# Performance work log

Measured on AMD Instinct MI355X. Metric: run time of the kernel, lower is better.

## Reference

```python
import jax, jax.numpy as jnp
import numpy as np

NUM_LAYERS = 5
EMB = 300
BN_EPS = 1e-5


def setup_inputs() -> dict:
    key = jax.random.key(0)
    ks = jax.random.split(key, 16)
    N, E, G = 50000, 800000, 512
    node_feats = jax.random.normal(ks[0], (N, EMB), dtype=jnp.float32)
    src = jax.random.randint(ks[1], (E,), 0, N, dtype=jnp.int32)
    dst = jax.random.randint(ks[2], (E,), 0, N, dtype=jnp.int32)
    graph_ids = jnp.sort(jax.random.randint(ks[3], (N,), 0, G, dtype=jnp.int32))
    L = NUM_LAYERS
    s1 = 1.0 / np.sqrt(EMB)
    s2 = 1.0 / np.sqrt(2 * EMB)
    W1 = jax.random.uniform(ks[4], (L, EMB, 2 * EMB), jnp.float32, -s1, s1)
    b1 = jax.random.uniform(ks[5], (L, 2 * EMB), jnp.float32, -s1, s1)
    W2 = jax.random.uniform(ks[6], (L, 2 * EMB, EMB), jnp.float32, -s2, s2)
    b2 = jax.random.uniform(ks[7], (L, EMB), jnp.float32, -s2, s2)
    eps = jnp.zeros((L,), dtype=jnp.float32)
    gamma = jnp.ones((L, EMB), dtype=jnp.float32)
    beta = jnp.zeros((L, EMB), dtype=jnp.float32)
    return {"node_feats": node_feats, "W1": W1, "b1": b1, "W2": W2, "b2": b2,
            "eps": eps, "gamma": gamma, "beta": beta,
            "src": src, "dst": dst, "graph_ids": graph_ids, "num_graphs": G}


def _batch_norm(x, g, b):
    mu = jnp.mean(x, axis=0)
    var = jnp.var(x, axis=0)
    return (x - mu) * jax.lax.rsqrt(var + BN_EPS) * g + b


def reference(node_feats, W1, b1, W2, b2, eps, gamma, beta, src, dst, graph_ids, num_graphs):
    N = node_feats.shape[0]
    h = node_feats
    for l in range(NUM_LAYERS):
        # message passing: sum of source-node feats at each destination
        neigh = jax.ops.segment_sum(h[src], dst, num_segments=N)  # [N, EMB]
        h = (1.0 + eps[l]) * h + neigh
        h = jax.nn.relu(h @ W1[l] + b1[l]) @ W2[l] + b2[l]
        h = _batch_norm(h, gamma[l], beta[l])
        if l < NUM_LAYERS - 1:
            h = jax.nn.relu(h)
        # dropout is identity in eval mode
    # JK='last' then mean readout per graph
    sums = jax.ops.segment_sum(h, graph_ids, num_segments=num_graphs)  # [G, EMB]
    cnt = jax.ops.segment_sum(jnp.ones((N,), h.dtype), graph_ids, num_segments=num_graphs)
    return sums / jnp.maximum(cnt, 1.0)[:, None]
```

## Files before the change

### kernel.cpp

```cpp
#include <hip/hip_runtime.h>
#include <hip/hip_bf16.h>
#include <stdint.h>

#define EMB 300
#define D1 320
#define D2 640
#define NLAYER 5

typedef __attribute__((ext_vector_type(8))) short short8v;
typedef __attribute__((ext_vector_type(4))) float f32x4;

__device__ __forceinline__ float bf2f(ushort u){
  union { uint32_t i; float f; } c; c.i = ((uint32_t)u) << 16; return c.f;
}
__device__ __forceinline__ ushort f2bf(float f){
  union { float f; uint32_t i; } c; c.f = f;
  uint32_t i = c.i;
  return (ushort)((i + 0x7FFFu + ((i >> 16) & 1u)) >> 16);
}

__global__ void k_prep_w1(const float* __restrict__ W1, ushort* __restrict__ W1H,
                          ushort* __restrict__ W1L){
  int id = blockIdx.x * 256 + threadIdx.x;
  if (id >= NLAYER * D2 * D1) return;
  int l = id / (D2 * D1), r = id % (D2 * D1);
  int n = r / D1, k = r % D1;
  float v = (n < 2*EMB && k < EMB) ? W1[((size_t)l * EMB + k) * (2*EMB) + n] : 0.f;
  ushort hi = f2bf(v);
  W1H[id] = hi;
  W1L[id] = f2bf(v - bf2f(hi));
}
__global__ void k_prep_w2(const float* __restrict__ W2, ushort* __restrict__ W2H,
                          ushort* __restrict__ W2L){
  int id = blockIdx.x * 256 + threadIdx.x;
  if (id >= NLAYER * D1 * D2) return;
  int l = id / (D1 * D2), r = id % (D1 * D2);
  int n = r / D2, k = r % D2;
  float v = (n < EMB && k < 2*EMB) ? W2[((size_t)l * (2*EMB) + k) * EMB + n] : 0.f;
  ushort hi = f2bf(v);
  W2H[id] = hi;
  W2L[id] = f2bf(v - bf2f(hi));
}
__global__ void k_prep_vec(const float* b1, const float* b2, const float* gamma, const float* beta,
                           float* b1p, float* b2p, float* gp, float* bp, float* scsh0){
  int id = blockIdx.x * 256 + threadIdx.x;
  if (id < NLAYER * D2){
    int l = id / D2, n = id % D2;
    b1p[id] = (n < 2*EMB) ? b1[l * (2*EMB) + n] : 0.f;
  }
  if (id < NLAYER * D1){
    int l = id / D1, c = id % D1;
    b2p[id] = (c < EMB) ? b2[l * EMB + c]    : 0.f;
    gp[id]  = (c < EMB) ? gamma[l * EMB + c] : 0.f;
    bp[id]  = (c < EMB) ? beta[l * EMB + c]  : 0.f;
  }
  if (id < D1){
    scsh0[id] = 1.0f;
    scsh0[D1 + id] = 0.0f;
  }
}
__global__ void k_hinit(const float* __restrict__ nf, float* __restrict__ z,
                        ushort* __restrict__ zbf, int N){
  int id = blockIdx.x * 256 + threadIdx.x;
  if (id >= N * 80) return;
  int n = id / 80, q = id % 80;
  float4 v = make_float4(0.f, 0.f, 0.f, 0.f);
  if (q < 75) v = *(const float4*)(nf + (size_t)n * EMB + q * 4);
  *(float4*)(z + (size_t)n * D1 + q * 4) = v;
  ushort o[4] = {f2bf(v.x), f2bf(v.y), f2bf(v.z), f2bf(v.w)};
  *(uint2*)(zbf + (size_t)n * D1 + q * 4) = *(const uint2*)o;
}

__global__ void k_count(const int* __restrict__ dst, int* __restrict__ deg, int E){
  int e = blockIdx.x * 256 + threadIdx.x;
  if (e < E) atomicAdd(&deg[dst[e]], 1);
}
__global__ __launch_bounds__(1024) void k_scan(const int* __restrict__ deg,
                                               int* __restrict__ row_ptr,
                                               int* __restrict__ cursor, int N){
  __shared__ int wsum[16];
  __shared__ int carryS;
  int tid = threadIdx.x, lane = tid & 63, wid = tid >> 6;
  if (tid == 0) carryS = 0;
  __syncthreads();
  for (int base = 0; base < N; base += 1024){
    int i = base + tid;
    int v = (i < N) ? deg[i] : 0;
    int isc = v;
    #pragma unroll
    for (int off = 1; off < 64; off <<= 1){
      int t = __shfl_up(isc, off, 64);
      if (lane >= off) isc += t;
    }
    if (lane == 63) wsum[wid] = isc;
    __syncthreads();
    int woff = 0;
    for (int ww = 0; ww < wid; ww++) woff += wsum[ww];
    int carry = carryS;
    int excl = carry + woff + isc - v;
    if (i < N){ row_ptr[i] = excl; cursor[i] = excl; }
    __syncthreads();
    if (tid == 0){
      int s = 0;
      for (int ww = 0; ww < 16; ww++) s += wsum[ww];
      carryS = carry + s;
    }
    __syncthreads();
  }
  if (tid == 0) row_ptr[N] = carryS;
}
__global__ void k_scatter(const int* __restrict__ src, const int* __restrict__ dst,
                          int* __restrict__ cursor, int* __restrict__ ssrc, int E){
  int e = blockIdx.x * 256 + threadIdx.x;
  if (e < E){
    int p = atomicAdd(&cursor[dst[e]], 1);
    ssrc[p] = src[e];
  }
}

__global__ __launch_bounds__(320) void k_aggregate(const float* __restrict__ z,
                                                   const ushort* __restrict__ zbf,
                                                   const float* __restrict__ scsh,
                                                   ushort* __restrict__ xh,
                                                   ushort* __restrict__ xl,
                                                   const int* __restrict__ row_ptr,
                                                   const int* __restrict__ ssrc,
                                                   const float* __restrict__ eps,
                                                   int l, int relu, int N){
  int t = threadIdx.x;
  int nl = t / 40, q = t % 40;
  int n = blockIdx.x * 8 + nl;
  if (n >= N) return;
  const int c0 = q * 8;
  float sc[8], sh[8];
  {
    float4 a = *(const float4*)(scsh + c0);
    float4 b = *(const float4*)(scsh + c0 + 4);
    float4 c = *(const float4*)(scsh + D1 + c0);
    float4 d = *(const float4*)(scsh + D1 + c0 + 4);
    sc[0]=a.x; sc[1]=a.y; sc[2]=a.z; sc[3]=a.w; sc[4]=b.x; sc[5]=b.y; sc[6]=b.z; sc[7]=b.w;
    sh[0]=c.x; sh[1]=c.y; sh[2]=c.z; sh[3]=c.w; sh[4]=d.x; sh[5]=d.y; sh[6]=d.z; sh[7]=d.w;
  }
  float acc[8];
  {
    const float* zp = z + (size_t)n * D1 + c0;
    float4 a = *(const float4*)zp, b = *(const float4*)(zp + 4);
    float v[8] = {a.x,a.y,a.z,a.w,b.x,b.y,b.z,b.w};
    float se = 1.0f + eps[l];
    #pragma unroll
    for (int j = 0; j < 8; j++){
      float u = fmaf(v[j], sc[j], sh[j]);
      if (relu) u = fmaxf(u, 0.f);
      acc[j] = se * u;
    }
  }
  auto accrow = [&](uint4 u){
    const ushort* us = (const ushort*)&u;
    #pragma unroll
    for (int j = 0; j < 8; j++){
      float x = fmaf(bf2f(us[j]), sc[j], sh[j]);
      if (relu) x = fmaxf(x, 0.f);
      acc[j] += x;
    }
  };
  int e0 = row_ptr[n], e1 = row_ptr[n + 1];
  int e = e0;
  for (; e + 4 <= e1; e += 4){
    int s0 = ssrc[e], s1 = ssrc[e+1], s2 = ssrc[e+2], s3 = ssrc[e+3];
    uint4 u0 = *(const uint4*)(zbf + (size_t)s0 * D1 + c0);
    uint4 u1 = *(const uint4*)(zbf + (size_t)s1 * D1 + c0);
    uint4 u2 = *(const uint4*)(zbf + (size_t)s2 * D1 + c0);
    uint4 u3 = *(const uint4*)(zbf + (size_t)s3 * D1 + c0);
    accrow(u0); accrow(u1); accrow(u2); accrow(u3);
  }
  for (; e < e1; e++){
    uint4 u = *(const uint4*)(zbf + (size_t)ssrc[e] * D1 + c0);
    accrow(u);
  }
  ushort oh[8], ol[8];
  #pragma unroll
  for (int j = 0; j < 8; j++){
    oh[j] = f2bf(acc[j]);
    ol[j] = f2bf(acc[j] - bf2f(oh[j]));
  }
  *(uint4*)(xh + (size_t)n * D1 + q * 8) = *(const uint4*)oh;
  *(uint4*)(xl + (size_t)n * D1 + q * 8) = *(const uint4*)ol;
}

template<int K, int LDC, int NBN, bool RELU, bool OUTSPLIT, bool STATS>
__global__ __launch_bounds__(256) void k_gemm(const ushort* __restrict__ AH,
                                              const ushort* __restrict__ AL,
                                              const ushort* __restrict__ BH,
                                              const ushort* __restrict__ BL,
                                              const float* __restrict__ bias,
                                              ushort* __restrict__ outh,
                                              ushort* __restrict__ outl,
                                              float* __restrict__ outf,
                                              ushort* __restrict__ outz,
                                              float* __restrict__ bnacc,
                                              int Nrows){
  __shared__ ushort smem[2 * 256 * 32 + 2 * 64 * 32];
  const int tid = threadIdx.x;
  const int lane = tid & 63;
  const int w = tid >> 6;

  const int nwg = gridDim.x;
  const int q8 = nwg >> 3, r8 = nwg & 7;
  const int xcd = blockIdx.x & 7, pos = blockIdx.x >> 3;
  const int wg = (xcd < r8 ? xcd * (q8 + 1) : r8 * (q8 + 1) + (xcd - r8) * q8) + pos;
  const size_t bm = (size_t)(wg / NBN) * 256;
  const int bn = (wg % NBN) * 64;

  f32x4 acc[4][4];
  #pragma unroll
  for (int m = 0; m < 4; m++)
    #pragma unroll
    for (int n = 0; n < 4; n++)
      acc[m][n] = f32x4{0.f, 0.f, 0.f, 0.f};

  ushort* lAh = smem;
  ushort* lAl = smem + 256 * 32;
  ushort* lBh = smem + 2 * 256 * 32;
  ushort* lBl = smem + 2 * 256 * 32 + 64 * 32;
  const int rsub = lane >> 2;
  const int gsw  = (lane & 3) ^ ((lane >> 4) & 3);
  const int csub = gsw * 8;

  for (int k0 = 0; k0 < K; k0 += 32){
    #pragma unroll
    for (int i = 0; i < 4; i++){
      int r = i * 64 + w * 16 + rsub;
      const ushort* gh = AH + (bm + r) * K + k0 + csub;
      const ushort* gl = AL + (bm + r) * K + k0 + csub;
      ushort* lph = lAh + (i * 64 + w * 16) * 32;
      ushort* lpl = lAl + (i * 64 + w * 16) * 32;
      __builtin_amdgcn_global_load_lds((const __attribute__((address_space(1))) void*)gh,
                                       (__attribute__((address_space(3))) void*)lph, 16, 0, 0);
      __builtin_amdgcn_global_load_lds((const __attribute__((address_space(1))) void*)gl,
                                       (__attribute__((address_space(3))) void*)lpl, 16, 0, 0);
    }
    {
      int r = w * 16 + rsub;
      const ushort* gh = BH + (size_t)(bn + r) * K + k0 + csub;
      const ushort* gl = BL + (size_t)(bn + r) * K + k0 + csub;
      ushort* lph = lBh + (w * 16) * 32;
      ushort* lpl = lBl + (w * 16) * 32;
      __builtin_amdgcn_global_load_lds((const __attribute__((address_space(1))) void*)gh,
                                       (__attribute__((address_space(3))) void*)lph, 16, 0, 0);
      __builtin_amdgcn_global_load_lds((const __attribute__((address_space(1))) void*)gl,
                                       (__attribute__((address_space(3))) void*)lpl, 16, 0, 0);
    }
    __syncthreads();
    short8v ah[4], al[4], bh[4], bl[4];
    const int kg = lane >> 4;
    const int mrow = lane & 15;
    const int krow = (kg ^ (mrow >> 2)) * 8;
    #pragma unroll
    for (int m = 0; m < 4; m++){
      ah[m] = *(const short8v*)(lAh + (w * 64 + m * 16 + mrow) * 32 + krow);
      al[m] = *(const short8v*)(lAl + (w * 64 + m * 16 + mrow) * 32 + krow);
    }
    #pragma unroll
    for (int n = 0; n < 4; n++){
      bh[n] = *(const short8v*)(lBh + (n * 16 + mrow) * 32 + krow);
      bl[n] = *(const short8v*)(lBl + (n * 16 + mrow) * 32 + krow);
    }
    #pragma unroll
    for (int m = 0; m < 4; m++)
      #pragma unroll
      for (int n = 0; n < 4; n++){
        acc[m][n] = __builtin_amdgcn_mfma_f32_16x16x32_bf16(al[m], bh[n], acc[m][n], 0, 0, 0);
        acc[m][n] = __builtin_amdgcn_mfma_f32_16x16x32_bf16(ah[m], bl[n], acc[m][n], 0, 0, 0);
        acc[m][n] = __builtin_amdgcn_mfma_f32_16x16x32_bf16(ah[m], bh[n], acc[m][n], 0, 0, 0);
      }
    __syncthreads();
  }

  float s1[4], s2[4];
  #pragma unroll
  for (int n = 0; n < 4; n++){ s1[n] = 0.f; s2[n] = 0.f; }

  const size_t rbase = bm + w * 64 + ((lane >> 4) * 4);
  #pragma unroll
  for (int n = 0; n < 4; n++){
    int c = bn + n * 16 + (lane & 15);
    float bv = bias[c];
    #pragma unroll
    for (int m = 0; m < 4; m++){
      #pragma unroll
      for (int j = 0; j < 4; j++){
        size_t r = rbase + m * 16 + j;
        float v = acc[m][n][j] + bv;
        if (RELU) v = fmaxf(v, 0.f);
        if (OUTSPLIT){
          ushort hi = f2bf(v);
          outh[r * LDC + c] = hi;
          outl[r * LDC + c] = f2bf(v - bf2f(hi));
        }
        if (STATS){
          outf[r * LDC + c] = v;
          outz[r * LDC + c] = f2bf(v);
          if (r < (size_t)Nrows){ s1[n] += v; s2[n] += v * v; }
        }
      }
    }
  }

  if (STATS){
    __shared__ float sred[2][64];
    if (tid < 64){ sred[0][tid] = 0.f; sred[1][tid] = 0.f; }
    __syncthreads();
    #pragma unroll
    for (int n = 0; n < 4; n++){
      float a = s1[n], b = s2[n];
      a += __shfl_xor(a, 16, 64); b += __shfl_xor(b, 16, 64);
      a += __shfl_xor(a, 32, 64); b += __shfl_xor(b, 32, 64);
      if (lane < 16){
        atomicAdd(&sred[0][n * 16 + lane], a);
        atomicAdd(&sred[1][n * 16 + lane], b);
      }
    }
    __syncthreads();
    if (tid < 64){
      atomicAdd(&bnacc[bn + tid], sred[0][tid]);
      atomicAdd(&bnacc[D1 + bn + tid], sred[1][tid]);
    }
  }
}

__global__ void k_bnfin(const float* __restrict__ accu, const float* __restrict__ gp,
                        const float* __restrict__ bp, int l, float* __restrict__ scsh, int N){
  int c = threadIdx.x;
  if (c >= D1) return;
  float invN = 1.0f / (float)N;
  float mu = accu[c] * invN;
  float var = accu[D1 + c] * invN - mu * mu;
  var = fmaxf(var, 0.f);
  float sc = gp[l * D1 + c] * rsqrtf(var + 1e-5f);
  scsh[c] = sc;
  scsh[D1 + c] = bp[l * D1 + c] - mu * sc;
}

__device__ __forceinline__ int lbound(const int* a, int n, int v){
  int lo = 0, hi = n;
  while (lo < hi){
    int mid = (lo + hi) >> 1;
    if (a[mid] < v) lo = mid + 1; else hi = mid;
  }
  return lo;
}
__global__ __launch_bounds__(128) void k_readout(const float* __restrict__ z,
                                                 const float* __restrict__ scsh,
                                                 const int* __restrict__ gid,
                                                 float* __restrict__ out, int N){
  int g = blockIdx.x;
  int t = threadIdx.x;
  if (t >= 75) return;
  int s = lbound(gid, N, g);
  int e = lbound(gid, N, g + 1);
  float a0 = 0.f, a1 = 0.f, a2 = 0.f, a3 = 0.f;
  int r = s;
  for (; r + 2 <= e; r += 2){
    float4 v0 = *(const float4*)(z + (size_t)r * D1 + t * 4);
    float4 v1 = *(const float4*)(z + (size_t)(r + 1) * D1 + t * 4);
    a0 += v0.x + v1.x; a1 += v0.y + v1.y; a2 += v0.z + v1.z; a3 += v0.w + v1.w;
  }
  if (r < e){
    float4 v = *(const float4*)(z + (size_t)r * D1 + t * 4);
    a0 += v.x; a1 += v.y; a2 += v.z; a3 += v.w;
  }
  int c = t * 4;
  int cnt = e - s;
  if (cnt <= 0){
    out[(size_t)g * EMB + c + 0] = 0.f;
    out[(size_t)g * EMB + c + 1] = 0.f;
    out[(size_t)g * EMB + c + 2] = 0.f;
    out[(size_t)g * EMB + c + 3] = 0.f;
    return;
  }
  float inv = 1.0f / (float)cnt;
  float4 sc = *(const float4*)(scsh + c);
  float4 sh = *(const float4*)(scsh + D1 + c);
  out[(size_t)g * EMB + c + 0] = fmaf(a0 * inv, sc.x, sh.x);
  out[(size_t)g * EMB + c + 1] = fmaf(a1 * inv, sc.y, sh.y);
  out[(size_t)g * EMB + c + 2] = fmaf(a2 * inv, sc.z, sh.z);
  out[(size_t)g * EMB + c + 3] = fmaf(a3 * inv, sc.w, sh.w);
}

extern "C" void kernel_launch(void* const* d_in, const int* in_sizes, int n_in,
                              void* d_out, int out_size, void* d_ws, size_t ws_size,
                              hipStream_t stream){
  const float* node_feats = (const float*)d_in[0];
  const float* W1    = (const float*)d_in[1];
  const float* b1    = (const float*)d_in[2];
  const float* W2    = (const float*)d_in[3];
  const float* b2    = (const float*)d_in[4];
  const float* eps   = (const float*)d_in[5];
  const float* gamma = (const float*)d_in[6];
  const float* beta  = (const float*)d_in[7];
  const int* src = (const int*)d_in[8];
  const int* dst = (const int*)d_in[9];
  const int* gid = (const int*)d_in[10];

  const int N = in_sizes[0] / EMB;
  const int E = in_sizes[8];
  const int G = out_size / EMB;
  const int MPAD = ((N + 255) / 256) * 256;

  char* ws = (char*)d_ws;
  const size_t seg = (size_t)MPAD * D1 * 4;
  char* S0 = ws;
  char* S1 = ws + seg;
  char* S2 = ws + 2 * seg;

  size_t off = 3 * seg;
  auto alloc = [&](size_t b){ size_t o = off; off += (b + 255) & ~(size_t)255; return o; };
  ushort* zbf  = (ushort*)(ws + alloc((size_t)MPAD * D1 * 2));
  ushort* w1h  = (ushort*)(ws + alloc((size_t)NLAYER * D2 * D1 * 2));
  ushort* w1l  = (ushort*)(ws + alloc((size_t)NLAYER * D2 * D1 * 2));
  ushort* w2h  = (ushort*)(ws + alloc((size_t)NLAYER * D1 * D2 * 2));
  ushort* w2l  = (ushort*)(ws + alloc((size_t)NLAYER * D1 * D2 * 2));
  float* b1p = (float*)(ws + alloc(NLAYER * D2 * 4));
  float* b2p = (float*)(ws + alloc(NLAYER * D1 * 4));
  float* gp  = (float*)(ws + alloc(NLAYER * D1 * 4));
  float* bp  = (float*)(ws + alloc(NLAYER * D1 * 4));
  int* deg     = (int*)(ws + alloc((size_t)N * 4));
  int* row_ptr = (int*)(ws + alloc((size_t)(N + 1) * 4));
  int* cursor  = (int*)(ws + alloc((size_t)N * 4));
  int* ssrc    = (int*)(ws + alloc((size_t)E * 4));
  float* bnacc = (float*)(ws + alloc(2 * D1 * 4));
  float* scsh  = (float*)(ws + alloc(2 * D1 * 4));
  float* scsh0 = (float*)(ws + alloc(2 * D1 * 4));

  k_prep_w1<<<(NLAYER * D2 * D1 + 255) / 256, 256, 0, stream>>>(W1, w1h, w1l);
  k_prep_w2<<<(NLAYER * D1 * D2 + 255) / 256, 256, 0, stream>>>(W2, w2h, w2l);
  k_prep_vec<<<(NLAYER * D2 + 255) / 256, 256, 0, stream>>>(b1, b2, gamma, beta,
                                                            b1p, b2p, gp, bp, scsh0);
  k_hinit<<<((size_t)N * 80 + 255) / 256, 256, 0, stream>>>(node_feats, (float*)S0, zbf, N);

  hipMemsetAsync(deg, 0, (size_t)N * 4, stream);
  k_count<<<(E + 255) / 256, 256, 0, stream>>>(dst, deg, E);
  k_scan<<<1, 1024, 0, stream>>>(deg, row_ptr, cursor, N);
  k_scatter<<<(E + 255) / 256, 256, 0, stream>>>(src, dst, cursor, ssrc, E);

  for (int l = 0; l < NLAYER; l++){
    char* zin  = (l & 1) ? S1 : S0;
    char* xsg  = (l & 1) ? S0 : S1;
    ushort* xh = (ushort*)xsg;
    ushort* xl = xh + (size_t)MPAD * D1;
    ushort* yh = (ushort*)zin;
    ushort* yl = (ushort*)S2;
    float* zout = (float*)xsg;
    const float* scin = (l == 0) ? scsh0 : scsh;

    k_aggregate<<<(N + 7) / 8, 320, 0, stream>>>((const float*)zin, zbf, scin, xh, xl,
                                                 row_ptr, ssrc, eps, l, (l > 0) ? 1 : 0, N);
    k_gemm<D1, D2, D2/64, true, true, false><<<(MPAD / 256) * (D2 / 64), 256, 0, stream>>>(
        xh, xl, w1h + (size_t)l * D2 * D1, w1l + (size_t)l * D2 * D1,
        b1p + l * D2, yh, yl, nullptr, nullptr, nullptr, 0);
    hipMemsetAsync(bnacc, 0, 2 * D1 * 4, stream);
    k_gemm<D2, D1, D1/64, false, false, true><<<(MPAD / 256) * (D1 / 64), 256, 0, stream>>>(
        yh, yl, w2h + (size_t)l * D1 * D2, w2l + (size_t)l * D1 * D2,
        b2p + l * D1, nullptr, nullptr, zout, zbf, bnacc, N);
    k_bnfin<<<1, D1, 0, stream>>>(bnacc, gp, bp, l, scsh, N);
  }
  k_readout<<<G, 128, 0, stream>>>((const float*)S1, scsh, gid, (float*)d_out, N);
}
```

Measured before the change: 1.643 ms.

## Double-buffer GEMM LDS tiles and store layer output as bf16 hi/lo pairs

The GEMM main loop now uses two LDS buffers, so the global-to-LDS load of the next K tile is issued before the MFMAs on the current tile, overlapping memory with compute. Layer outputs are no longer written as an fp32 array plus a separate bf16 copy; the second GEMM writes a bf16 hi/lo split that aggregate and readout read back. This removes one output write stream, but neighbor gathers now use only the hi part, and LDS use per block doubles, which may lower occupancy.

```diff
diff --git a/kernel.cpp b/kernel.cpp
--- a/kernel.cpp
+++ b/kernel.cpp
@@ -59,16 +59,22 @@
     scsh0[D1 + id] = 0.0f;
   }
 }
-__global__ void k_hinit(const float* __restrict__ nf, float* __restrict__ z,
-                        ushort* __restrict__ zbf, int N){
+__global__ void k_hinit(const float* __restrict__ nf, ushort* __restrict__ zh,
+                        ushort* __restrict__ zl, int N){
   int id = blockIdx.x * 256 + threadIdx.x;
   if (id >= N * 80) return;
   int n = id / 80, q = id % 80;
   float4 v = make_float4(0.f, 0.f, 0.f, 0.f);
   if (q < 75) v = *(const float4*)(nf + (size_t)n * EMB + q * 4);
-  *(float4*)(z + (size_t)n * D1 + q * 4) = v;
-  ushort o[4] = {f2bf(v.x), f2bf(v.y), f2bf(v.z), f2bf(v.w)};
-  *(uint2*)(zbf + (size_t)n * D1 + q * 4) = *(const uint2*)o;
+  float vv[4] = {v.x, v.y, v.z, v.w};
+  ushort hh[4], hl[4];
+  #pragma unroll
+  for (int j = 0; j < 4; j++){
+    hh[j] = f2bf(vv[j]);
+    hl[j] = f2bf(vv[j] - bf2f(hh[j]));
+  }
+  *(uint2*)(zh + (size_t)n * D1 + q * 4) = *(const uint2*)hh;
+  *(uint2*)(zl + (size_t)n * D1 + q * 4) = *(const uint2*)hl;
 }
 
 __global__ void k_count(const int* __restrict__ dst, int* __restrict__ deg, int E){
@@ -118,8 +124,8 @@
   }
 }
 
-__global__ __launch_bounds__(320) void k_aggregate(const float* __restrict__ z,
-                                                   const ushort* __restrict__ zbf,
+__global__ __launch_bounds__(320) void k_aggregate(const ushort* __restrict__ zh,
+                                                   const ushort* __restrict__ zl,
                                                    const float* __restrict__ scsh,
                                                    ushort* __restrict__ xh,
                                                    ushort* __restrict__ xl,
@@ -143,13 +149,15 @@
   }
   float acc[8];
   {
-    const float* zp = z + (size_t)n * D1 + c0;
-    float4 a = *(const float4*)zp, b = *(const float4*)(zp + 4);
-    float v[8] = {a.x,a.y,a.z,a.w,b.x,b.y,b.z,b.w};
+    uint4 uh = *(const uint4*)(zh + (size_t)n * D1 + c0);
+    uint4 ul = *(const uint4*)(zl + (size_t)n * D1 + c0);
+    const ushort* ph = (const ushort*)&uh;
+    const ushort* pl = (const ushort*)&ul;
     float se = 1.0f + eps[l];
     #pragma unroll
     for (int j = 0; j < 8; j++){
-      float u = fmaf(v[j], sc[j], sh[j]);
+      float v = bf2f(ph[j]) + bf2f(pl[j]);
+      float u = fmaf(v, sc[j], sh[j]);
       if (relu) u = fmaxf(u, 0.f);
       acc[j] = se * u;
     }
@@ -167,14 +175,14 @@
   int e = e0;
   for (; e + 4 <= e1; e += 4){
     int s0 = ssrc[e], s1 = ssrc[e+1], s2 = ssrc[e+2], s3 = ssrc[e+3];
-    uint4 u0 = *(const uint4*)(zbf + (size_t)s0 * D1 + c0);
-    uint4 u1 = *(const uint4*)(zbf + (size_t)s1 * D1 + c0);
-    uint4 u2 = *(const uint4*)(zbf + (size_t)s2 * D1 + c0);
-    uint4 u3 = *(const uint4*)(zbf + (size_t)s3 * D1 + c0);
+    uint4 u0 = *(const uint4*)(zh + (size_t)s0 * D1 + c0);
+    uint4 u1 = *(const uint4*)(zh + (size_t)s1 * D1 + c0);
+    uint4 u2 = *(const uint4*)(zh + (size_t)s2 * D1 + c0);
+    uint4 u3 = *(const uint4*)(zh + (size_t)s3 * D1 + c0);
     accrow(u0); accrow(u1); accrow(u2); accrow(u3);
   }
   for (; e < e1; e++){
-    uint4 u = *(const uint4*)(zbf + (size_t)ssrc[e] * D1 + c0);
+    uint4 u = *(const uint4*)(zh + (size_t)ssrc[e] * D1 + c0);
     accrow(u);
   }
   ushort oh[8], ol[8];
@@ -187,7 +195,7 @@
   *(uint4*)(xl + (size_t)n * D1 + q * 8) = *(const uint4*)ol;
 }
 
-template<int K, int LDC, int NBN, bool RELU, bool OUTSPLIT, bool STATS>
+template<int K, int LDC, int NBN, bool RELU, bool STATS>
 __global__ __launch_bounds__(256) void k_gemm(const ushort* __restrict__ AH,
                                               const ushort* __restrict__ AL,
                                               const ushort* __restrict__ BH,
@@ -195,11 +203,9 @@
                                               const float* __restrict__ bias,
                                               ushort* __restrict__ outh,
                                               ushort* __restrict__ outl,
-                                              float* __restrict__ outf,
-                                              ushort* __restrict__ outz,
                                               float* __restrict__ bnacc,
                                               int Nrows){
-  __shared__ ushort smem[2 * 256 * 32 + 2 * 64 * 32];
+  __shared__ ushort smem[2 * 20480];
   const int tid = threadIdx.x;
   const int lane = tid & 63;
   const int w = tid >> 6;
@@ -218,22 +224,19 @@
     for (int n = 0; n < 4; n++)
       acc[m][n] = f32x4{0.f, 0.f, 0.f, 0.f};
 
-  ushort* lAh = smem;
-  ushort* lAl = smem + 256 * 32;
-  ushort* lBh = smem + 2 * 256 * 32;
-  ushort* lBl = smem + 2 * 256 * 32 + 64 * 32;
   const int rsub = lane >> 2;
   const int gsw  = (lane & 3) ^ ((lane >> 4) & 3);
   const int csub = gsw * 8;
 
-  for (int k0 = 0; k0 < K; k0 += 32){
+  auto stage = [&](int buf, int k0){
+    ushort* base = smem + buf * 20480;
     #pragma unroll
     for (int i = 0; i < 4; i++){
       int r = i * 64 + w * 16 + rsub;
       const ushort* gh = AH + (bm + r) * K + k0 + csub;
       const ushort* gl = AL + (bm + r) * K + k0 + csub;
-      ushort* lph = lAh + (i * 64 + w * 16) * 32;
-      ushort* lpl = lAl + (i * 64 + w * 16) * 32;
+      ushort* lph = base + (i * 64 + w * 16) * 32;
+      ushort* lpl = base + 8192 + (i * 64 + w * 16) * 32;
       __builtin_amdgcn_global_load_lds((const __attribute__((address_space(1))) void*)gh,
                                        (__attribute__((address_space(3))) void*)lph, 16, 0, 0);
       __builtin_amdgcn_global_load_lds((const __attribute__((address_space(1))) void*)gl,
@@ -243,27 +246,35 @@
       int r = w * 16 + rsub;
       const ushort* gh = BH + (size_t)(bn + r) * K + k0 + csub;
       const ushort* gl = BL + (size_t)(bn + r) * K + k0 + csub;
-      ushort* lph = lBh + (w * 16) * 32;
-      ushort* lpl = lBl + (w * 16) * 32;
+      ushort* lph = base + 16384 + (w * 16) * 32;
+      ushort* lpl = base + 18432 + (w * 16) * 32;
       __builtin_amdgcn_global_load_lds((const __attribute__((address_space(1))) void*)gh,
                                        (__attribute__((address_space(3))) void*)lph, 16, 0, 0);
       __builtin_amdgcn_global_load_lds((const __attribute__((address_space(1))) void*)gl,
                                        (__attribute__((address_space(3))) void*)lpl, 16, 0, 0);
     }
-    __syncthreads();
+  };
+
+  const int NT = K / 32;
+  stage(0, 0);
+  __syncthreads();
+  int cur = 0;
+  for (int t = 0; t < NT; t++){
+    if (t + 1 < NT) stage(cur ^ 1, (t + 1) * 32);
+    ushort* base = smem + cur * 20480;
     short8v ah[4], al[4], bh[4], bl[4];
     const int kg = lane >> 4;
     const int mrow = lane & 15;
     const int krow = (kg ^ (mrow >> 2)) * 8;
     #pragma unroll
     for (int m = 0; m < 4; m++){
-      ah[m] = *(const short8v*)(lAh + (w * 64 + m * 16 + mrow) * 32 + krow);
-      al[m] = *(const short8v*)(lAl + (w * 64 + m * 16 + mrow) * 32 + krow);
+      ah[m] = *(const short8v*)(base + (w * 64 + m * 16 + mrow) * 32 + krow);
+      al[m] = *(const short8v*)(base + 8192 + (w * 64 + m * 16 + mrow) * 32 + krow);
     }
     #pragma unroll
     for (int n = 0; n < 4; n++){
-      bh[n] = *(const short8v*)(lBh + (n * 16 + mrow) * 32 + krow);
-      bl[n] = *(const short8v*)(lBl + (n * 16 + mrow) * 32 + krow);
+      bh[n] = *(const short8v*)(base + 16384 + (n * 16 + mrow) * 32 + krow);
+      bl[n] = *(const short8v*)(base + 18432 + (n * 16 + mrow) * 32 + krow);
     }
     #pragma unroll
     for (int m = 0; m < 4; m++)
@@ -274,6 +285,7 @@
         acc[m][n] = __builtin_amdgcn_mfma_f32_16x16x32_bf16(ah[m], bh[n], acc[m][n], 0, 0, 0);
       }
     __syncthreads();
+    cur ^= 1;
   }
 
   float s1[4], s2[4];
@@ -292,14 +304,10 @@
         size_t r = rbase + m * 16 + j;
         float v = acc[m][n][j] + bv;
         if (RELU) v = fmaxf(v, 0.f);
-        if (OUTSPLIT){
-          ushort hi = f2bf(v);
-          outh[r * LDC + c] = hi;
-          outl[r * LDC + c] = f2bf(v - bf2f(hi));
-        }
+        ushort hi = f2bf(v);
+        outh[r * LDC + c] = hi;
+        outl[r * LDC + c] = f2bf(v - bf2f(hi));
         if (STATS){
-          outf[r * LDC + c] = v;
-          outz[r * LDC + c] = f2bf(v);
           if (r < (size_t)Nrows){ s1[n] += v; s2[n] += v * v; }
         }
       }
@@ -307,8 +315,8 @@
   }
 
   if (STATS){
-    __shared__ float sred[2][64];
-    if (tid < 64){ sred[0][tid] = 0.f; sred[1][tid] = 0.f; }
+    float* sred = (float*)smem;
+    if (tid < 128) sred[tid] = 0.f;
     __syncthreads();
     #pragma unroll
     for (int n = 0; n < 4; n++){
@@ -316,14 +324,14 @@
       a += __shfl_xor(a, 16, 64); b += __shfl_xor(b, 16, 64);
       a += __shfl_xor(a, 32, 64); b += __shfl_xor(b, 32, 64);
       if (lane < 16){
-        atomicAdd(&sred[0][n * 16 + lane], a);
-        atomicAdd(&sred[1][n * 16 + lane], b);
+        atomicAdd(&sred[n * 16 + lane], a);
+        atomicAdd(&sred[64 + n * 16 + lane], b);
       }
     }
     __syncthreads();
     if (tid < 64){
-      atomicAdd(&bnacc[bn + tid], sred[0][tid]);
-      atomicAdd(&bnacc[D1 + bn + tid], sred[1][tid]);
+      atomicAdd(&bnacc[bn + tid], sred[tid]);
+      atomicAdd(&bnacc[D1 + bn + tid], sred[64 + tid]);
     }
   }
 }
@@ -349,7 +357,8 @@
   }
   return lo;
 }
-__global__ __launch_bounds__(128) void k_readout(const float* __restrict__ z,
+__global__ __launch_bounds__(128) void k_readout(const ushort* __restrict__ zh,
+                                                 const ushort* __restrict__ zl,
                                                  const float* __restrict__ scsh,
                                                  const int* __restrict__ gid,
                                                  float* __restrict__ out, int N){
@@ -359,15 +368,15 @@
   int s = lbound(gid, N, g);
   int e = lbound(gid, N, g + 1);
   float a0 = 0.f, a1 = 0.f, a2 = 0.f, a3 = 0.f;
-  int r = s;
-  for (; r + 2 <= e; r += 2){
-    float4 v0 = *(const float4*)(z + (size_t)r * D1 + t * 4);
-    float4 v1 = *(const float4*)(z + (size_t)(r + 1) * D1 + t * 4);
-    a0 += v0.x + v1.x; a1 += v0.y + v1.y; a2 += v0.z + v1.z; a3 += v0.w + v1.w;
-  }
-  if (r < e){
-    float4 v = *(const float4*)(z + (size_t)r * D1 + t * 4);
-    a0 += v.x; a1 += v.y; a2 += v.z; a3 += v.w;
+  for (int r = s; r < e; r++){
+    uint2 uh = *(const uint2*)(zh + (size_t)r * D1 + t * 4);
+    uint2 ul = *(const uint2*)(zl + (size_t)r * D1 + t * 4);
+    const ushort* ph = (const ushort*)&uh;
+    const ushort* pl = (const ushort*)&ul;
+    a0 += bf2f(ph[0]) + bf2f(pl[0]);
+    a1 += bf2f(ph[1]) + bf2f(pl[1]);
+    a2 += bf2f(ph[2]) + bf2f(pl[2]);
+    a3 += bf2f(ph[3]) + bf2f(pl[3]);
   }
   int c = t * 4;
   int cnt = e - s;
@@ -408,14 +417,14 @@
   const int MPAD = ((N + 255) / 256) * 256;
 
   char* ws = (char*)d_ws;
-  const size_t seg = (size_t)MPAD * D1 * 4;
+  const size_t seg  = (size_t)MPAD * D1 * 4;
+  const size_t half = (size_t)MPAD * D1;
   char* S0 = ws;
   char* S1 = ws + seg;
   char* S2 = ws + 2 * seg;
 
   size_t off = 3 * seg;
   auto alloc = [&](size_t b){ size_t o = off; off += (b + 255) & ~(size_t)255; return o; };
-  ushort* zbf  = (ushort*)(ws + alloc((size_t)MPAD * D1 * 2));
   ushort* w1h  = (ushort*)(ws + alloc((size_t)NLAYER * D2 * D1 * 2));
   ushort* w1l  = (ushort*)(ws + alloc((size_t)NLAYER * D2 * D1 * 2));
   ushort* w2h  = (ushort*)(ws + alloc((size_t)NLAYER * D1 * D2 * 2));
@@ -436,7 +445,8 @@
   k_prep_w2<<<(NLAYER * D1 * D2 + 255) / 256, 256, 0, stream>>>(W2, w2h, w2l);
   k_prep_vec<<<(NLAYER * D2 + 255) / 256, 256, 0, stream>>>(b1, b2, gamma, beta,
                                                             b1p, b2p, gp, bp, scsh0);
-  k_hinit<<<((size_t)N * 80 + 255) / 256, 256, 0, stream>>>(node_feats, (float*)S0, zbf, N);
+  k_hinit<<<((size_t)N * 80 + 255) / 256, 256, 0, stream>>>(node_feats,
+                                                            (ushort*)S0, (ushort*)S0 + half, N);
 
   hipMemsetAsync(deg, 0, (size_t)N * 4, stream);
   k_count<<<(E + 255) / 256, 256, 0, stream>>>(dst, deg, E);
@@ -446,23 +456,27 @@
   for (int l = 0; l < NLAYER; l++){
     char* zin  = (l & 1) ? S1 : S0;
     char* xsg  = (l & 1) ? S0 : S1;
+    ushort* zh = (ushort*)zin;
+    ushort* zl = zh + half;
     ushort* xh = (ushort*)xsg;
-    ushort* xl = xh + (size_t)MPAD * D1;
+    ushort* xl = xh + half;
     ushort* yh = (ushort*)zin;
     ushort* yl = (ushort*)S2;
-    float* zout = (float*)xsg;
+    ushort* zoh = (ushort*)xsg;
+    ushort* zol = zoh + half;
     const float* scin = (l == 0) ? scsh0 : scsh;
 
-    k_aggregate<<<(N + 7) / 8, 320, 0, stream>>>((const float*)zin, zbf, scin, xh, xl,
+    k_aggregate<<<(N + 7) / 8, 320, 0, stream>>>(zh, zl, scin, xh, xl,
                                                  row_ptr, ssrc, eps, l, (l > 0) ? 1 : 0, N);
-    k_gemm<D1, D2, D2/64, true, true, false><<<(MPAD / 256) * (D2 / 64), 256, 0, stream>>>(
+    k_gemm<D1, D2, D2/64, true, false><<<(MPAD / 256) * (D2 / 64), 256, 0, stream>>>(
         xh, xl, w1h + (size_t)l * D2 * D1, w1l + (size_t)l * D2 * D1,
-        b1p + l * D2, yh, yl, nullptr, nullptr, nullptr, 0);
+        b1p + l * D2, yh, yl, nullptr, 0);
     hipMemsetAsync(bnacc, 0, 2 * D1 * 4, stream);
-    k_gemm<D2, D1, D1/64, false, false, true><<<(MPAD / 256) * (D1 / 64), 256, 0, stream>>>(
+    k_gemm<D2, D1, D1/64, false, true><<<(MPAD / 256) * (D1 / 64), 256, 0, stream>>>(
         yh, yl, w2h + (size_t)l * D1 * D2, w2l + (size_t)l * D1 * D2,
-        b2p + l * D1, nullptr, nullptr, zout, zbf, bnacc, N);
+        b2p + l * D1, zoh, zol, bnacc, N);
     k_bnfin<<<1, D1, 0, stream>>>(bnacc, gp, bp, l, scsh, N);
   }
-  k_readout<<<G, 128, 0, stream>>>((const float*)S1, scsh, gid, (float*)d_out, N);
-}
+  k_readout<<<G, 128, 0, stream>>>((ushort*)S1, (ushort*)S1 + half, scsh, gid,
+                                   (float*)d_out, N);
+}
```

Result: faster. 1.562 ms (-4.9%).
